# Kernel tuning notes

Hardware: AMD Instinct MI355X
Metric: run time of the kernel (lower is better)

## Reference

```python
import jax, jax.numpy as jnp
import numpy as np

B = 32768
SF = 40  # subframe_size


def _gru_cell(x, h, wih, whh):
    # PyTorch GRUCell (bias=False): gates ordered [r; z; n]
    gi = x @ wih.T
    gh = h @ whh.T
    ir, iz, inn = jnp.split(gi, 3, axis=-1)
    hr, hz, hn = jnp.split(gh, 3, axis=-1)
    r = jax.nn.sigmoid(ir + hr)
    z = jax.nn.sigmoid(iz + hz)
    n = jnp.tanh(inn + r * hn)
    return (1.0 - z) * n + z * h


def setup_inputs() -> dict:
    key = jax.random.key(0)
    ks = iter(jax.random.split(key, 32))

    def rn(shape, scale=None):
        s = scale if scale is not None else 1.0 / np.sqrt(shape[-1])
        return (jax.random.normal(next(ks), shape, dtype=jnp.float32) * s)

    inp = {
        'cond': rn((B, 80), 1.0),
        'prev_pred': rn((B, 256), 1.0),
        'exc_mem': rn((B, 256), 1.0),
        'period': 32.0 + 223.0 * jax.random.uniform(next(ks), (B,), dtype=jnp.float32),
        's1': rn((B, 160), 1.0),
        's2': rn((B, 128), 1.0),
        's3': rn((B, 128), 1.0),
        's4': rn((B, 164), 1.0),
        'w_gain': rn((1, 80)),
        'b_gain': jnp.zeros((1,), jnp.float32),
        'w_fwc0': rn((192, 328)),
        'w_fwc0_glu': rn((192, 192)),
        'wih1': rn((480, 272)),
        'whh1': rn((480, 160)),
        'wglu1': rn((160, 160)),
        'wih2': rn((384, 240)),
        'whh2': rn((384, 128)),
        'wglu2': rn((128, 128)),
        'wih3': rn((384, 208)),
        'whh3': rn((384, 128)),
        'wglu3': rn((128, 128)),
        'w_skip': rn((128, 688)),
        'w_skip_glu': rn((128, 128)),
        'w_sig': rn((40, 128)),
        'w_pg': rn((4, 192)),
        'b_pg': jnp.zeros((4,), jnp.float32),
    }
    return inp


def reference(cond, prev_pred, exc_mem, period, s1, s2, s3, s4,
              w_gain, b_gain, w_fwc0, w_fwc0_glu,
              wih1, whh1, wglu1, wih2, whh2, wglu2, wih3, whh3, wglu3,
              w_skip, w_skip_glu, w_sig, w_pg, b_pg):
    # eval mode (training=False): quantization noise is identity; compat_mode=False path
    dt = cond.dtype
    period = jnp.clip(jnp.nan_to_num(period, nan=128.0, posinf=128.0, neginf=128.0), 32.0, 255.0)
    rng = jnp.arange(SF + 4, dtype=dt)
    # fractional pitch lookup with linear interpolation into exc_mem
    idxf = 256.0 - period[:, None] + rng[None, :] - 2.0  # [B, SF+4]
    idx0 = jnp.floor(idxf)
    alpha = jnp.clip(idxf - idx0, 0.0, 1.0)
    W = exc_mem.shape[1]
    i0 = jnp.mod(jnp.clip(idx0, 0.0, 255.0).astype(jnp.int32), W)
    i1 = jnp.mod(jnp.clip(idx0 + 1.0, 0.0, 255.0).astype(jnp.int32), W)
    v0 = jnp.take_along_axis(exc_mem, i0, axis=1)
    v1 = jnp.take_along_axis(exc_mem, i1, axis=1)
    pred = (1.0 - alpha) * v0 + alpha * v1  # [B, SF+4]

    # bounded gain
    gain = 0.2 + 0.8 * jax.nn.sigmoid(cond @ w_gain.T + b_gain)
    gain = jnp.clip(jnp.nan_to_num(gain, nan=1.0, posinf=20.0, neginf=1e-3), 1e-3, 20.0)
    inv = 1.0 / (1e-5 + gain)
    pred_n = pred * inv
    prev = exc_mem[:, -SF:] * inv
    tmp = jnp.concatenate([cond, pred_n, prev], axis=1)  # [B, 164]
    fpitch = pred_n[:, 2:-2]  # [B, SF]

    # FWConv: linear over cat(state, x), tanh, GLU
    xcat = jnp.concatenate([s4, tmp], axis=1)  # [B, 328]
    fw = jnp.tanh(xcat @ w_fwc0.T)
    fwc0_out = fw * jax.nn.sigmoid(fw @ w_fwc0_glu.T)  # [B, 192]
    new_s4 = tmp

    pitch_gain = jax.nn.sigmoid(fwc0_out @ w_pg.T + b_pg)  # [B, 4]

    h1 = _gru_cell(jnp.concatenate([fwc0_out, pitch_gain[:, 0:1] * fpitch, prev], 1), s1, wih1, whh1)
    g1 = h1 * jax.nn.sigmoid(h1 @ wglu1.T)
    h2 = _gru_cell(jnp.concatenate([g1, pitch_gain[:, 1:2] * fpitch, prev], 1), s2, wih2, whh2)
    g2 = h2 * jax.nn.sigmoid(h2 @ wglu2.T)
    h3 = _gru_cell(jnp.concatenate([g2, pitch_gain[:, 2:3] * fpitch, prev], 1), s3, wih3, whh3)
    g3 = h3 * jax.nn.sigmoid(h3 @ wglu3.T)

    skip_in = jnp.concatenate([g1, g2, g3, fwc0_out, pitch_gain[:, 3:4] * fpitch, prev], 1)  # [B, 688]
    sk = jnp.tanh(skip_in @ w_skip.T)
    sk = sk * jax.nn.sigmoid(sk @ w_skip_glu.T)
    sig_out = jnp.tanh(sk @ w_sig.T) * gain  # [B, SF]

    exc_mem_new = jnp.concatenate([exc_mem[:, SF:], sig_out], 1)
    prev_pred_new = jnp.concatenate([prev_pred[:, SF:], pred[:, 2:2 + SF]], 1)
    return sig_out, exc_mem_new, prev_pred_new, h1, h2, h3, new_s4
```

## Files before the change

kernel.cpp:

```cpp
#include <hip/hip_runtime.h>
#include <hip/hip_bf16.h>
#include <cstdint>
#include <cmath>

#define BTOT 32768L
#define OSIG 0L
#define OEXC (BTOT*40L)
#define OPREV (OEXC + BTOT*256L)
#define OH1 (OPREV + BTOT*256L)
#define OH2 (OH1 + BTOT*160L)
#define OH3 (OH2 + BTOT*128L)
#define ONS4 (OH3 + BTOT*128L)

typedef __attribute__((ext_vector_type(8))) short short8;
typedef __attribute__((ext_vector_type(4))) short short4v;
typedef __attribute__((ext_vector_type(4))) float f32x4;

#define AP 968

#define W_F0     0L
#define W_F0G    67584L
#define W_PG     104448L
#define W_IH1R   107520L
#define W_IH1Z   162816L
#define W_IH1N   218112L
#define W_HH1R   273408L
#define W_HH1Z   310272L
#define W_HH1N   347136L
#define W_GLU1   384000L
#define W_IH2R   420864L
#define W_IH2Z   453632L
#define W_IH2N   486400L
#define W_HH2R   519168L
#define W_HH2Z   535552L
#define W_HH2N   551936L
#define W_GLU2   568320L
#define W_IH3R   584704L
#define W_IH3Z   613376L
#define W_IH3N   642048L
#define W_HH3R   670720L
#define W_HH3Z   687104L
#define W_HH3N   703488L
#define W_GLU3   719872L
#define W_SKIP   736256L
#define W_SKIPG  859136L
#define W_SIG    875520L

__device__ __forceinline__ float sigm(float x){ return 1.0f/(1.0f+__expf(-x)); }
__device__ __forceinline__ float tanh_f(float x){
    float e = __expf(2.0f*x);
    return 1.0f - 2.0f/(e+1.0f);
}
__device__ __forceinline__ uint16_t f2bf(float x){
    __hip_bfloat16 h = __float2bfloat16(x);
    return *(uint16_t*)&h;
}
__device__ __forceinline__ float bf2f(uint16_t h){
    union { float f; uint32_t u; } v; v.u = ((uint32_t)h)<<16;
    return v.f;
}
__device__ __forceinline__ short4v pack4(float4 v){
    short4v r;
    r.x=(short)f2bf(v.x); r.y=(short)f2bf(v.y); r.z=(short)f2bf(v.z); r.w=(short)f2bf(v.w);
    return r;
}

struct PrepArgs { const float* s[15]; };

__global__ __launch_bounds__(64) void prep_kernel(PrepArgs pa, uint16_t* dst){
    static const long J[27][8] = {
        {0,  0,192,328,352,192, W_F0,   0},
        {1,  0,192,192,192,192, W_F0G,  0},
        {13, 0,  4,192,192, 16, W_PG,   0},
        {2,  0,160,272,288,192, W_IH1R, 0},
        {2,160,160,272,288,192, W_IH1Z, 0},
        {2,320,160,272,288,192, W_IH1N, 0},
        {3,  0,160,160,192,192, W_HH1R, 0},
        {3,160,160,160,192,192, W_HH1Z, 0},
        {3,320,160,160,192,192, W_HH1N, 0},
        {4,  0,160,160,192,192, W_GLU1, 0},
        {5,  0,128,240,256,128, W_IH2R, 0},
        {5,128,128,240,256,128, W_IH2Z, 0},
        {5,256,128,240,256,128, W_IH2N, 0},
        {6,  0,128,128,128,128, W_HH2R, 0},
        {6,128,128,128,128,128, W_HH2Z, 0},
        {6,256,128,128,128,128, W_HH2N, 0},
        {7,  0,128,128,128,128, W_GLU2, 0},
        {8,  0,128,208,224,128, W_IH3R, 0},
        {8,128,128,208,224,128, W_IH3Z, 0},
        {8,256,128,208,224,128, W_IH3N, 0},
        {9,  0,128,128,128,128, W_HH3R, 0},
        {9,128,128,128,128,128, W_HH3Z, 0},
        {9,256,128,128,128,128, W_HH3N, 0},
        {10, 0,128,128,128,128, W_GLU3, 0},
        {11, 0,128,688,960,128, W_SKIP, 1},
        {12, 0,128,128,128,128, W_SKIPG,0},
        {14, 0, 40,128,128, 64, W_SIG,  0},
    };
    long row = blockIdx.x;
    int j = 0;
    while (row >= J[j][5]) { row -= J[j][5]; ++j; }
    const float* src = pa.s[J[j][0]];
    const long ro = J[j][1], N = J[j][2], K = J[j][3], KP = J[j][4];
    const int type = (int)J[j][7];
    uint16_t* d = dst + J[j][6] + row*KP;
    for (long k = threadIdx.x; k < KP; k += 64){
        float v = 0.0f;
        if (row < N){
            if (type == 0){
                if (k < K) v = src[(ro+row)*K + k];
            } else {
                long s = -1;
                if (k < 192) s = 416 + k;
                else if (k >= 232 && k < 272) s = 648 + (k-232);
                else if (k >= 288 && k < 448) s = (k-288);
                else if (k >= 544 && k < 672) s = 160 + (k-544);
                else if (k >= 768 && k < 896) s = 288 + (k-768);
                else if (k >= 896 && k < 936) s = 608 + (k-896);
                if (s >= 0) v = src[row*688 + s];
            }
        }
        d[k] = f2bf(v);
    }
}

template<int KS, int CNT>
__device__ __forceinline__ void wgemm4(f32x4 (&acc)[CNT][2],
    const uint16_t* __restrict__ Bw, int KP,
    const uint16_t* A, int P, int w, int r16, int g)
{
    constexpr int T = KS*CNT;
    constexpr int PF = (T < 6) ? T : 6;
    const uint16_t* ap = A + r16*P + g*8;
    const uint16_t* bbase = Bw + (size_t)(w*16 + r16)*KP + g*8;
    short8 ring[PF];
    #pragma unroll
    for (int t=0;t<PF;++t)
        ring[t] = *(const short8*)(bbase + (size_t)(t%CNT)*64*KP + (size_t)(t/CNT)*32);
    short8 af[2];
    #pragma unroll
    for (int t=0;t<T;++t){
        const int s = t/CNT, i = t%CNT;
        if (i==0){
            #pragma unroll
            for (int mt=0;mt<2;++mt) af[mt] = *(const short8*)(ap + mt*16*P + s*32);
        }
        short8 bf = ring[t%PF];
        if (t+PF < T)
            ring[t%PF] = *(const short8*)(bbase + (size_t)((t+PF)%CNT)*64*KP + (size_t)((t+PF)/CNT)*32);
        #pragma unroll
        for (int mt=0;mt<2;++mt)
            acc[i][mt] = __builtin_amdgcn_mfma_f32_16x16x32_bf16(af[mt], bf, acc[i][mt],0,0,0);
    }
}
template<int CNT> __device__ __forceinline__ void zacc(f32x4 (&a)[CNT][2]){
    f32x4 z4 = {0.f,0.f,0.f,0.f};
    #pragma unroll
    for (int i=0;i<CNT;++i){
        #pragma unroll
        for (int mt=0;mt<2;++mt) a[i][mt]=z4;
    }
}

__device__ __forceinline__ void gru1_h(const uint16_t* __restrict__ W, uint16_t* ACTp,
    const float* __restrict__ s1g, float* __restrict__ out,
    float (&hk)[3][2][4], int row0, int w, int r16, int g)
{
    f32x4 gx[3][2], gh[3][2], ra[3][2], za[3][2];
    zacc(gx); zacc(gh); zacc(ra); zacc(za);
    wgemm4<9,3>(gx, W+W_IH1N, 288, ACTp,     AP, w,r16,g);
    wgemm4<9,3>(ra, W+W_IH1R, 288, ACTp,     AP, w,r16,g);
    wgemm4<9,3>(za, W+W_IH1Z, 288, ACTp,     AP, w,r16,g);
    wgemm4<6,3>(gh, W+W_HH1N, 192, ACTp+544, AP, w,r16,g);
    wgemm4<6,3>(ra, W+W_HH1R, 192, ACTp+544, AP, w,r16,g);
    wgemm4<6,3>(za, W+W_HH1Z, 192, ACTp+544, AP, w,r16,g);
    #pragma unroll
    for (int i=0;i<3;++i){
        int n = (w+4*i)*16 + r16;
        #pragma unroll
        for (int mt=0;mt<2;++mt){
            #pragma unroll
            for (int q=0;q<4;++q){
                int mrow = mt*16+g*4+q;
                float h = 0.f;
                if (n < 160){
                    float hpv = s1g[(long)(row0+mrow)*160 + n];
                    float r = sigm(ra[i][mt][q]);
                    float z = sigm(za[i][mt][q]);
                    float nn = tanh_f(gx[i][mt][q] + r*gh[i][mt][q]);
                    h = (1.f-z)*nn + z*hpv;
                    out[OH1 + (long)(row0+mrow)*160 + n] = h;
                }
                hk[i][mt][q] = h;
                ACTp[mrow*AP+768+n] = f2bf(h);
            }
        }
    }
}
__device__ __forceinline__ void glu1(const uint16_t* __restrict__ W, uint16_t* ACTp,
                                     float (&hk)[3][2][4], int w, int r16, int g){
    f32x4 gl[3][2];
    zacc(gl);
    wgemm4<6,3>(gl, W+W_GLU1, 192, ACTp+768, AP, w,r16,g);
    #pragma unroll
    for (int i=0;i<3;++i){
        int n = (w+4*i)*16 + r16;
        if (n < 160){
            #pragma unroll
            for (int mt=0;mt<2;++mt)
                #pragma unroll
                for (int q=0;q<4;++q){
                    int mrow = mt*16+g*4+q;
                    ACTp[mrow*AP + 288 + n] = f2bf(hk[i][mt][q]*sigm(gl[i][mt][q]));
                }
        }
    }
}

template<int KSX, int KSH>
__device__ __forceinline__ void gru23_h(
    const uint16_t* __restrict__ Wxr, const uint16_t* __restrict__ Wxz, const uint16_t* __restrict__ Wxn, int KPX,
    const uint16_t* __restrict__ Whr, const uint16_t* __restrict__ Whz, const uint16_t* __restrict__ Whn, int KPH,
    const uint16_t* XA, const uint16_t* HA, int HAP,
    const float* __restrict__ sg, float* __restrict__ outp, long obase,
    uint16_t* HBdst, int HBpitch,
    float (&hk)[2][2][4], int row0, int w, int r16, int g)
{
    f32x4 gx[2][2], gh[2][2], ra[2][2], za[2][2];
    zacc(gx); zacc(gh); zacc(ra); zacc(za);
    wgemm4<KSX,2>(gx, Wxn, KPX, XA, AP, w,r16,g);
    wgemm4<KSX,2>(ra, Wxr, KPX, XA, AP, w,r16,g);
    wgemm4<KSX,2>(za, Wxz, KPX, XA, AP, w,r16,g);
    wgemm4<KSH,2>(gh, Whn, KPH, HA, HAP, w,r16,g);
    wgemm4<KSH,2>(ra, Whr, KPH, HA, HAP, w,r16,g);
    wgemm4<KSH,2>(za, Whz, KPH, HA, HAP, w,r16,g);
    #pragma unroll
    for (int i=0;i<2;++i){
        int n = (w+4*i)*16 + r16;
        #pragma unroll
        for (int mt=0;mt<2;++mt){
            #pragma unroll
            for (int q=0;q<4;++q){
                int mrow = mt*16+g*4+q;
                float hpv = sg[(long)(row0+mrow)*128 + n];
                float r = sigm(ra[i][mt][q]), z = sigm(za[i][mt][q]);
                float nn = tanh_f(gx[i][mt][q] + r*gh[i][mt][q]);
                float h = (1.f-z)*nn + z*hpv;
                outp[obase + (long)(row0+mrow)*128 + n] = h;
                hk[i][mt][q] = h;
                if (HBdst) HBdst[mrow*HBpitch + n] = f2bf(h);
            }
        }
    }
}

extern "C" __global__ __launch_bounds__(256, 2)
void fargan_mfma(const float* __restrict__ cond, const float* __restrict__ prev_pred,
                 const float* __restrict__ exc_mem, const float* __restrict__ period,
                 const float* __restrict__ s1, const float* __restrict__ s2,
                 const float* __restrict__ s3, const float* __restrict__ s4,
                 const float* __restrict__ w_gain, const float* __restrict__ b_gain,
                 const float* __restrict__ b_pg,
                 const uint16_t* __restrict__ W, float* __restrict__ out)
{
    __shared__ __align__(16) uint16_t ACT[32*AP];
    __shared__ __align__(16) uint16_t SH[32*136];
    __shared__ uint16_t FPITCHb[32*40];
    __shared__ float GAIN[32];
    __shared__ float PGs[32][4];

    const int tid = threadIdx.x;
    const int row0 = blockIdx.x * 32;
    const int w = tid >> 6, l = tid & 63, r16 = l & 15, g = l >> 4;
    const int rr = tid >> 3, c8 = tid & 7;
    const long grow = row0 + rr;

    const float* exc_row = exc_mem + grow*256;

    float a0 = 0.f;
    {
        const float4* c4 = (const float4*)(cond + grow*80);
        const float4* g4 = (const float4*)w_gain;
        float4* on4 = (float4*)(out + ONS4 + grow*164);
        for (int i=c8;i<20;i+=8){
            float4 cv = c4[i], gv = g4[i];
            a0 += cv.x*gv.x + cv.y*gv.y + cv.z*gv.z + cv.w*gv.w;
            *(short4v*)&ACT[rr*AP + 164 + 4*i] = pack4(cv);
            on4[i] = cv;
        }
    }
    a0 += __shfl_xor(a0,4,8); a0 += __shfl_xor(a0,2,8); a0 += __shfl_xor(a0,1,8);
    float gn = 0.2f + 0.8f*sigm(a0 + b_gain[0]);
    if (!(gn==gn)) gn = 1.0f;
    gn = fminf(fmaxf(gn, 0.001f), 20.0f);
    float inv = 1.0f/(1e-5f+gn);
    if (c8==0) GAIN[rr] = gn;

    float p = period[grow];
    p = (fabsf(p) <= 3.0e38f) ? p : 128.0f;
    p = fminf(fmaxf(p, 32.0f), 255.0f);

    for (int e=c8;e<44;e+=8){
        float idxf = 254.0f - p + (float)e;
        float idx0 = floorf(idxf);
        float al = fminf(fmaxf(idxf-idx0, 0.f), 1.f);
        int i0 = (int)fminf(fmaxf(idx0, 0.f), 255.f);
        int i1 = (int)fminf(fmaxf(idx0+1.f, 0.f), 255.f);
        float pr = (1.f-al)*exc_row[i0] + al*exc_row[i1];
        float pn = pr*inv;
        ACT[rr*AP + 244 + e] = f2bf(pn);
        out[ONS4 + grow*164 + 80 + e] = pn;
        if (e>=2 && e<42){
            out[OPREV + grow*256 + 216 + (e-2)] = pr;
            FPITCHb[rr*40 + (e-2)] = f2bf(pn);
        }
    }
    {
        const float4* pv4 = (const float4*)(exc_row + 216);
        float4* onp = (float4*)(out + ONS4 + grow*164 + 124);
        for (int i=c8;i<10;i+=8){
            float4 v = pv4[i];
            v.x*=inv; v.y*=inv; v.z*=inv; v.w*=inv;
            *(short4v*)&ACT[rr*AP + 288 + 4*i] = pack4(v);
            onp[i] = v;
        }
    }
    {
        const float4* s44 = (const float4*)(s4 + grow*164);
        for (int i=c8;i<41;i+=8)
            *(short4v*)&ACT[rr*AP + 4*i] = pack4(s44[i]);
        const float4* s14 = (const float4*)(s1 + grow*160);
        for (int i=c8;i<40;i+=8)
            *(short4v*)&ACT[rr*AP + 544 + 4*i] = pack4(s14[i]);
    }
    for (int i=328+c8;i<352;i+=8) ACT[rr*AP + i] = 0;
    for (int i=704+c8;i<736;i+=8) ACT[rr*AP + i] = 0;
    {
        const float4* pp4 = (const float4*)(prev_pred + grow*256 + 40);
        const float4* ex4 = (const float4*)(exc_row + 40);
        float4* op4 = (float4*)(out + OPREV + grow*256);
        float4* oe4 = (float4*)(out + OEXC + grow*256);
        for (int i=c8;i<54;i+=8){ op4[i] = pp4[i]; oe4[i] = ex4[i]; }
    }
    __syncthreads();

    float fwk[3][2][4];

    {
        f32x4 av[3][2]; zacc(av);
        wgemm4<11,3>(av, W+W_F0, 352, ACT, AP, w,r16,g);
        #pragma unroll
        for (int i=0;i<3;++i){
            int n = (w+4*i)*16 + r16;
            #pragma unroll
            for (int mt=0;mt<2;++mt)
                #pragma unroll
                for (int q=0;q<4;++q){
                    int mrow = mt*16+g*4+q;
                    float t = tanh_f(av[i][mt][q]);
                    fwk[i][mt][q] = t;
                    ACT[mrow*AP+352+n] = f2bf(t);
                }
        }
    }
    __syncthreads();

    {
        f32x4 av[3][2]; zacc(av);
        wgemm4<6,3>(av, W+W_F0G, 192, ACT+352, AP, w,r16,g);
        #pragma unroll
        for (int i=0;i<3;++i){
            int n = (w+4*i)*16 + r16;
            #pragma unroll
            for (int mt=0;mt<2;++mt)
                #pragma unroll
                for (int q=0;q<4;++q){
                    int mrow = mt*16+g*4+q;
                    ACT[mrow*AP+n] = f2bf(fwk[i][mt][q]*sigm(av[i][mt][q]));
                }
        }
    }
    __syncthreads();

    {
        f32x4 av[1][2]; zacc(av);
        wgemm4<6,1>(av, W+W_PG, 192, ACT, AP, 0, r16, g);
        if (w==0 && r16<4){
            float bp = b_pg[r16];
            #pragma unroll
            for (int mt=0;mt<2;++mt)
                #pragma unroll
                for (int q=0;q<4;++q)
                    PGs[mt*16+g*4+q][r16] = sigm(av[0][mt][q] + bp);
        }
    }
    __syncthreads();

    for (int i=c8;i<40;i+=8){
        ACT[rr*AP+192+i] = f2bf(PGs[rr][0]*bf2f(FPITCHb[rr*40+i]));
        ACT[rr*AP+232+i] = ACT[rr*AP+288+i];
    }
    __syncthreads();

    float hk1[3][2][4];
    gru1_h(W, ACT, s1, out, hk1, row0, w,r16,g);
    __syncthreads();

    glu1(W, ACT, hk1, w,r16,g);
    {
        const float4* s24 = (const float4*)(s2 + grow*128);
        for (int i=c8;i<32;i+=8)
            *(short4v*)&ACT[rr*AP + 544 + 4*i] = pack4(s24[i]);
    }
    for (int i=c8;i<40;i+=8){
        ACT[rr*AP+448+i] = f2bf(PGs[rr][1]*bf2f(FPITCHb[rr*40+i]));
        ACT[rr*AP+488+i] = ACT[rr*AP+232+i];
    }
    for (int i=528+c8;i<544;i+=8) ACT[rr*AP+i] = 0;
    __syncthreads();

    float hk[2][2][4];
    gru23_h<8,4>(W+W_IH2R, W+W_IH2Z, W+W_IH2N, 256,
                 W+W_HH2R, W+W_HH2Z, W+W_HH2N, 128,
                 ACT+288, ACT+544, AP, s2, out, OH2,
                 ACT+768, AP, hk, row0, w,r16,g);
    __syncthreads();

    {
        f32x4 gl[2][2]; zacc(gl);
        wgemm4<4,2>(gl, W+W_GLU2, 128, ACT+768, AP, w,r16,g);
        #pragma unroll
        for (int i=0;i<2;++i){
            int n = (w+4*i)*16 + r16;
            #pragma unroll
            for (int mt=0;mt<2;++mt)
                #pragma unroll
                for (int q=0;q<4;++q){
                    int mrow = mt*16+g*4+q;
                    ACT[mrow*AP+544+n] = f2bf(hk[i][mt][q]*sigm(gl[i][mt][q]));
                }
        }
    }
    {
        const float4* s34 = (const float4*)(s3 + grow*128);
        for (int i=c8;i<32;i+=8)
            *(short4v*)&SH[rr*136 + 4*i] = pack4(s34[i]);
    }
    for (int i=c8;i<40;i+=8){
        ACT[rr*AP+672+i] = f2bf(PGs[rr][2]*bf2f(FPITCHb[rr*40+i]));
        ACT[rr*AP+712+i] = ACT[rr*AP+232+i];
    }
    for (int i=752+c8;i<768;i+=8) ACT[rr*AP+i] = 0;
    __syncthreads();

    gru23_h<7,4>(W+W_IH3R, W+W_IH3Z, W+W_IH3N, 224,
                 W+W_HH3R, W+W_HH3Z, W+W_HH3N, 128,
                 ACT+544, SH, 136, s3, out, OH3,
                 (uint16_t*)nullptr, 0, hk, row0, w,r16,g);
    __syncthreads();

    #pragma unroll
    for (int i=0;i<2;++i){
        int n = (w+4*i)*16 + r16;
        #pragma unroll
        for (int mt=0;mt<2;++mt)
            #pragma unroll
            for (int q=0;q<4;++q)
                SH[(mt*16+g*4+q)*136 + n] = f2bf(hk[i][mt][q]);
    }
    __syncthreads();

    {
        f32x4 gl[2][2]; zacc(gl);
        wgemm4<4,2>(gl, W+W_GLU3, 128, SH, 136, w,r16,g);
        #pragma unroll
        for (int i=0;i<2;++i){
            int n = (w+4*i)*16 + r16;
            #pragma unroll
            for (int mt=0;mt<2;++mt)
                #pragma unroll
                for (int q=0;q<4;++q){
                    int mrow = mt*16+g*4+q;
                    ACT[mrow*AP+768+n] = f2bf(hk[i][mt][q]*sigm(gl[i][mt][q]));
                }
        }
    }
    for (int i=c8;i<40;i+=8)
        ACT[rr*AP+896+i] = f2bf(PGs[rr][3]*bf2f(FPITCHb[rr*40+i]));
    __syncthreads();

    float skk[2][2][4];
    {
        f32x4 av[2][2]; zacc(av);
        wgemm4<30,2>(av, W+W_SKIP, 960, ACT, AP, w,r16,g);
        #pragma unroll
        for (int i=0;i<2;++i){
            int n = (w+4*i)*16 + r16;
            #pragma unroll
            for (int mt=0;mt<2;++mt)
                #pragma unroll
                for (int q=0;q<4;++q){
                    int mrow = mt*16+g*4+q;
                    float t = tanh_f(av[i][mt][q]);
                    skk[i][mt][q] = t;
                    SH[mrow*136+n] = f2bf(t);
                }
        }
    }
    __syncthreads();
    {
        f32x4 av[2][2]; zacc(av);
        wgemm4<4,2>(av, W+W_SKIPG, 128, SH, 136, w,r16,g);
        #pragma unroll
        for (int i=0;i<2;++i){
            int n = (w+4*i)*16 + r16;
            #pragma unroll
            for (int mt=0;mt<2;++mt)
                #pragma unroll
                for (int q=0;q<4;++q){
                    int mrow = mt*16+g*4+q;
                    ACT[mrow*AP+n] = f2bf(skk[i][mt][q]*sigm(av[i][mt][q]));
                }
        }
    }
    __syncthreads();
    {
        f32x4 av[1][2]; zacc(av);
        wgemm4<4,1>(av, W+W_SIG, 128, ACT, AP, w,r16,g);
        int n = w*16 + r16;
        if (n < 40){
            #pragma unroll
            for (int mt=0;mt<2;++mt)
                #pragma unroll
                for (int q=0;q<4;++q){
                    int mrow = mt*16+g*4+q;
                    float sv = tanh_f(av[0][mt][q]) * GAIN[mrow];
                    out[OSIG + (long)(row0+mrow)*40 + n] = sv;
                    out[OEXC + (long)(row0+mrow)*256 + 216 + n] = sv;
                }
        }
    }
}

extern "C" void kernel_launch(void* const* d_in, const int* in_sizes, int n_in,
                              void* d_out, int out_size, void* d_ws, size_t ws_size,
                              hipStream_t stream) {
    const float* cond      = (const float*)d_in[0];
    const float* prev_pred = (const float*)d_in[1];
    const float* exc_mem   = (const float*)d_in[2];
    const float* period    = (const float*)d_in[3];
    const float* s1        = (const float*)d_in[4];
    const float* s2        = (const float*)d_in[5];
    const float* s3        = (const float*)d_in[6];
    const float* s4        = (const float*)d_in[7];
    const float* w_gain    = (const float*)d_in[8];
    const float* b_gain    = (const float*)d_in[9];
    const float* w_fwc0    = (const float*)d_in[10];
    const float* w_fwc0_glu= (const float*)d_in[11];
    const float* wih1      = (const float*)d_in[12];
    const float* whh1      = (const float*)d_in[13];
    const float* wglu1     = (const float*)d_in[14];
    const float* wih2      = (const float*)d_in[15];
    const float* whh2      = (const float*)d_in[16];
    const float* wglu2     = (const float*)d_in[17];
    const float* wih3      = (const float*)d_in[18];
    const float* whh3      = (const float*)d_in[19];
    const float* wglu3     = (const float*)d_in[20];
    const float* w_skip    = (const float*)d_in[21];
    const float* w_skip_glu= (const float*)d_in[22];
    const float* w_sig     = (const float*)d_in[23];
    const float* w_pg      = (const float*)d_in[24];
    const float* b_pg      = (const float*)d_in[25];
    float* out = (float*)d_out;
    uint16_t* wsbf = (uint16_t*)d_ws;

    PrepArgs pa;
    pa.s[0]=w_fwc0; pa.s[1]=w_fwc0_glu; pa.s[2]=wih1; pa.s[3]=whh1; pa.s[4]=wglu1;
    pa.s[5]=wih2; pa.s[6]=whh2; pa.s[7]=wglu2; pa.s[8]=wih3; pa.s[9]=whh3;
    pa.s[10]=wglu3; pa.s[11]=w_skip; pa.s[12]=w_skip_glu; pa.s[13]=w_pg; pa.s[14]=w_sig;

    hipLaunchKernelGGL(prep_kernel, dim3(3856), dim3(64), 0, stream, pa, wsbf);
    hipLaunchKernelGGL(fargan_mfma, dim3(1024), dim3(256), 0, stream,
        cond, prev_pred, exc_mem, period, s1, s2, s3, s4,
        w_gain, b_gain, b_pg, wsbf, out);
}
```

Baseline: 261.9 us.

## Switch to 32x32x16 MFMA with 64-row tiles and 512-thread blocks

Replaces the 16x16x32 MFMA GEMM helper with 32x32x16 bf16 MFMA tiles, doubles rows per block to 64 and threads to 512 (8 waves split by M-half and N-column). The three GRU gate GEMMs share one A-fragment load (wg3), and activations needed by the GLU steps are re-read from LDS instead of kept in registers. This is meant to halve weight traffic per row and raise MFMA efficiency. The cost is much larger LDS per block (about 130 KB), the loss of the B-prefetch ring, and uneven work across waves in the 192-wide stages.

```diff
diff --git a/kernel.cpp b/kernel.cpp
--- a/kernel.cpp
+++ b/kernel.cpp
@@ -14,37 +14,37 @@
 
 typedef __attribute__((ext_vector_type(8))) short short8;
 typedef __attribute__((ext_vector_type(4))) short short4v;
-typedef __attribute__((ext_vector_type(4))) float f32x4;
+typedef __attribute__((ext_vector_type(16))) float f32x16;
 
 #define AP 968
 
 #define W_F0     0L
 #define W_F0G    67584L
 #define W_PG     104448L
-#define W_IH1R   107520L
-#define W_IH1Z   162816L
-#define W_IH1N   218112L
-#define W_HH1R   273408L
-#define W_HH1Z   310272L
-#define W_HH1N   347136L
-#define W_GLU1   384000L
-#define W_IH2R   420864L
-#define W_IH2Z   453632L
-#define W_IH2N   486400L
-#define W_HH2R   519168L
-#define W_HH2Z   535552L
-#define W_HH2N   551936L
-#define W_GLU2   568320L
-#define W_IH3R   584704L
-#define W_IH3Z   613376L
-#define W_IH3N   642048L
-#define W_HH3R   670720L
-#define W_HH3Z   687104L
-#define W_HH3N   703488L
-#define W_GLU3   719872L
-#define W_SKIP   736256L
-#define W_SKIPG  859136L
-#define W_SIG    875520L
+#define W_IH1R   110592L
+#define W_IH1Z   165888L
+#define W_IH1N   221184L
+#define W_HH1R   276480L
+#define W_HH1Z   313344L
+#define W_HH1N   350208L
+#define W_GLU1   387072L
+#define W_IH2R   423936L
+#define W_IH2Z   456704L
+#define W_IH2N   489472L
+#define W_HH2R   522240L
+#define W_HH2Z   538624L
+#define W_HH2N   555008L
+#define W_GLU2   571392L
+#define W_IH3R   587776L
+#define W_IH3Z   616448L
+#define W_IH3N   645120L
+#define W_HH3R   673792L
+#define W_HH3Z   690176L
+#define W_HH3N   706560L
+#define W_GLU3   722944L
+#define W_SKIP   739328L
+#define W_SKIPG  862208L
+#define W_SIG    878592L
 
 __device__ __forceinline__ float sigm(float x){ return 1.0f/(1.0f+__expf(-x)); }
 __device__ __forceinline__ float tanh_f(float x){
@@ -64,6 +64,10 @@
     r.x=(short)f2bf(v.x); r.y=(short)f2bf(v.y); r.z=(short)f2bf(v.z); r.w=(short)f2bf(v.w);
     return r;
 }
+__device__ __forceinline__ void z16(f32x16 &a){
+    #pragma unroll
+    for (int i=0;i<16;++i) a[i]=0.f;
+}
 
 struct PrepArgs { const float* s[15]; };
 
@@ -71,7 +75,7 @@
     static const long J[27][8] = {
         {0,  0,192,328,352,192, W_F0,   0},
         {1,  0,192,192,192,192, W_F0G,  0},
-        {13, 0,  4,192,192, 16, W_PG,   0},
+        {13, 0,  4,192,192, 32, W_PG,   0},
         {2,  0,160,272,288,192, W_IH1R, 0},
         {2,160,160,272,288,192, W_IH1Z, 0},
         {2,320,160,272,288,192, W_IH1N, 0},
@@ -124,137 +128,51 @@
     }
 }
 
-template<int KS, int CNT>
-__device__ __forceinline__ void wgemm4(f32x4 (&acc)[CNT][2],
-    const uint16_t* __restrict__ Bw, int KP,
-    const uint16_t* A, int P, int w, int r16, int g)
+template<int KS, int NT>
+__device__ __forceinline__ void wg1(f32x16 (&acc)[NT],
+    const uint16_t* __restrict__ B, int KP,
+    const uint16_t* A, int P, int mt, int nb, int c32, int hl)
 {
-    constexpr int T = KS*CNT;
-    constexpr int PF = (T < 6) ? T : 6;
-    const uint16_t* ap = A + r16*P + g*8;
-    const uint16_t* bbase = Bw + (size_t)(w*16 + r16)*KP + g*8;
-    short8 ring[PF];
+    const uint16_t* ap = A + (mt*32 + c32)*P + hl*8;
+    const uint16_t* bp = B + (size_t)(nb + c32)*KP + hl*8;
     #pragma unroll
-    for (int t=0;t<PF;++t)
-        ring[t] = *(const short8*)(bbase + (size_t)(t%CNT)*64*KP + (size_t)(t/CNT)*32);
-    short8 af[2];
+    for (int s=0;s<KS;++s){
+        short8 a = *(const short8*)(ap + s*16);
+        #pragma unroll
+        for (int i=0;i<NT;++i){
+            short8 b = *(const short8*)(bp + (size_t)(i*128)*KP + s*16);
+            acc[i] = __builtin_amdgcn_mfma_f32_32x32x16_bf16(a, b, acc[i], 0,0,0);
+        }
+    }
+}
+template<int KS, int NT>
+__device__ __forceinline__ void wg3(f32x16 (&a0)[NT], f32x16 (&a1)[NT], f32x16 (&a2)[NT],
+    const uint16_t* __restrict__ B0, const uint16_t* __restrict__ B1,
+    const uint16_t* __restrict__ B2, int KP,
+    const uint16_t* A, int P, int mt, int nb, int c32, int hl)
+{
+    const uint16_t* ap = A + (mt*32 + c32)*P + hl*8;
+    const size_t boff = (size_t)(nb + c32)*KP + hl*8;
+    const uint16_t* b0 = B0 + boff;
+    const uint16_t* b1 = B1 + boff;
+    const uint16_t* b2 = B2 + boff;
     #pragma unroll
-    for (int t=0;t<T;++t){
-        const int s = t/CNT, i = t%CNT;
-        if (i==0){
-            #pragma unroll
-            for (int mt=0;mt<2;++mt) af[mt] = *(const short8*)(ap + mt*16*P + s*32);
-        }
-        short8 bf = ring[t%PF];
-        if (t+PF < T)
-            ring[t%PF] = *(const short8*)(bbase + (size_t)((t+PF)%CNT)*64*KP + (size_t)((t+PF)/CNT)*32);
-        #pragma unroll
-        for (int mt=0;mt<2;++mt)
-            acc[i][mt] = __builtin_amdgcn_mfma_f32_16x16x32_bf16(af[mt], bf, acc[i][mt],0,0,0);
-    }
-}
-template<int CNT> __device__ __forceinline__ void zacc(f32x4 (&a)[CNT][2]){
-    f32x4 z4 = {0.f,0.f,0.f,0.f};
-    #pragma unroll
-    for (int i=0;i<CNT;++i){
-        #pragma unroll
-        for (int mt=0;mt<2;++mt) a[i][mt]=z4;
-    }
-}
-
-__device__ __forceinline__ void gru1_h(const uint16_t* __restrict__ W, uint16_t* ACTp,
-    const float* __restrict__ s1g, float* __restrict__ out,
-    float (&hk)[3][2][4], int row0, int w, int r16, int g)
-{
-    f32x4 gx[3][2], gh[3][2], ra[3][2], za[3][2];
-    zacc(gx); zacc(gh); zacc(ra); zacc(za);
-    wgemm4<9,3>(gx, W+W_IH1N, 288, ACTp,     AP, w,r16,g);
-    wgemm4<9,3>(ra, W+W_IH1R, 288, ACTp,     AP, w,r16,g);
-    wgemm4<9,3>(za, W+W_IH1Z, 288, ACTp,     AP, w,r16,g);
-    wgemm4<6,3>(gh, W+W_HH1N, 192, ACTp+544, AP, w,r16,g);
-    wgemm4<6,3>(ra, W+W_HH1R, 192, ACTp+544, AP, w,r16,g);
-    wgemm4<6,3>(za, W+W_HH1Z, 192, ACTp+544, AP, w,r16,g);
-    #pragma unroll
-    for (int i=0;i<3;++i){
-        int n = (w+4*i)*16 + r16;
-        #pragma unroll
-        for (int mt=0;mt<2;++mt){
-            #pragma unroll
-            for (int q=0;q<4;++q){
-                int mrow = mt*16+g*4+q;
-                float h = 0.f;
-                if (n < 160){
-                    float hpv = s1g[(long)(row0+mrow)*160 + n];
-                    float r = sigm(ra[i][mt][q]);
-                    float z = sigm(za[i][mt][q]);
-                    float nn = tanh_f(gx[i][mt][q] + r*gh[i][mt][q]);
-                    h = (1.f-z)*nn + z*hpv;
-                    out[OH1 + (long)(row0+mrow)*160 + n] = h;
-                }
-                hk[i][mt][q] = h;
-                ACTp[mrow*AP+768+n] = f2bf(h);
-            }
-        }
-    }
-}
-__device__ __forceinline__ void glu1(const uint16_t* __restrict__ W, uint16_t* ACTp,
-                                     float (&hk)[3][2][4], int w, int r16, int g){
-    f32x4 gl[3][2];
-    zacc(gl);
-    wgemm4<6,3>(gl, W+W_GLU1, 192, ACTp+768, AP, w,r16,g);
-    #pragma unroll
-    for (int i=0;i<3;++i){
-        int n = (w+4*i)*16 + r16;
-        if (n < 160){
-            #pragma unroll
-            for (int mt=0;mt<2;++mt)
-                #pragma unroll
-                for (int q=0;q<4;++q){
-                    int mrow = mt*16+g*4+q;
-                    ACTp[mrow*AP + 288 + n] = f2bf(hk[i][mt][q]*sigm(gl[i][mt][q]));
-                }
-        }
-    }
-}
-
-template<int KSX, int KSH>
-__device__ __forceinline__ void gru23_h(
-    const uint16_t* __restrict__ Wxr, const uint16_t* __restrict__ Wxz, const uint16_t* __restrict__ Wxn, int KPX,
-    const uint16_t* __restrict__ Whr, const uint16_t* __restrict__ Whz, const uint16_t* __restrict__ Whn, int KPH,
-    const uint16_t* XA, const uint16_t* HA, int HAP,
-    const float* __restrict__ sg, float* __restrict__ outp, long obase,
-    uint16_t* HBdst, int HBpitch,
-    float (&hk)[2][2][4], int row0, int w, int r16, int g)
-{
-    f32x4 gx[2][2], gh[2][2], ra[2][2], za[2][2];
-    zacc(gx); zacc(gh); zacc(ra); zacc(za);
-    wgemm4<KSX,2>(gx, Wxn, KPX, XA, AP, w,r16,g);
-    wgemm4<KSX,2>(ra, Wxr, KPX, XA, AP, w,r16,g);
-    wgemm4<KSX,2>(za, Wxz, KPX, XA, AP, w,r16,g);
-    wgemm4<KSH,2>(gh, Whn, KPH, HA, HAP, w,r16,g);
-    wgemm4<KSH,2>(ra, Whr, KPH, HA, HAP, w,r16,g);
-    wgemm4<KSH,2>(za, Whz, KPH, HA, HAP, w,r16,g);
-    #pragma unroll
-    for (int i=0;i<2;++i){
-        int n = (w+4*i)*16 + r16;
-        #pragma unroll
-        for (int mt=0;mt<2;++mt){
-            #pragma unroll
-            for (int q=0;q<4;++q){
-                int mrow = mt*16+g*4+q;
-                float hpv = sg[(long)(row0+mrow)*128 + n];
-                float r = sigm(ra[i][mt][q]), z = sigm(za[i][mt][q]);
-                float nn = tanh_f(gx[i][mt][q] + r*gh[i][mt][q]);
-                float h = (1.f-z)*nn + z*hpv;
-                outp[obase + (long)(row0+mrow)*128 + n] = h;
-                hk[i][mt][q] = h;
-                if (HBdst) HBdst[mrow*HBpitch + n] = f2bf(h);
-            }
-        }
-    }
-}
-
-extern "C" __global__ __launch_bounds__(256, 2)
+    for (int s=0;s<KS;++s){
+        short8 a = *(const short8*)(ap + s*16);
+        #pragma unroll
+        for (int i=0;i<NT;++i){
+            const size_t o = (size_t)(i*128)*KP + s*16;
+            short8 f0 = *(const short8*)(b0 + o);
+            short8 f1 = *(const short8*)(b1 + o);
+            short8 f2 = *(const short8*)(b2 + o);
+            a0[i] = __builtin_amdgcn_mfma_f32_32x32x16_bf16(a, f0, a0[i], 0,0,0);
+            a1[i] = __builtin_amdgcn_mfma_f32_32x32x16_bf16(a, f1, a1[i], 0,0,0);
+            a2[i] = __builtin_amdgcn_mfma_f32_32x32x16_bf16(a, f2, a2[i], 0,0,0);
+        }
+    }
+}
+
+extern "C" __global__ __launch_bounds__(512, 2)
 void fargan_mfma(const float* __restrict__ cond, const float* __restrict__ prev_pred,
                  const float* __restrict__ exc_mem, const float* __restrict__ period,
                  const float* __restrict__ s1, const float* __restrict__ s2,
@@ -263,15 +181,17 @@
                  const float* __restrict__ b_pg,
                  const uint16_t* __restrict__ W, float* __restrict__ out)
 {
-    __shared__ __align__(16) uint16_t ACT[32*AP];
-    __shared__ __align__(16) uint16_t SH[32*136];
-    __shared__ uint16_t FPITCHb[32*40];
-    __shared__ float GAIN[32];
-    __shared__ float PGs[32][4];
+    __shared__ __align__(16) uint16_t ACT[64*AP];
+    __shared__ __align__(16) uint16_t SH[64*136];
+    __shared__ uint16_t FPITCHb[64*40];
+    __shared__ float GAIN[64];
+    __shared__ float PGs[64][4];
 
     const int tid = threadIdx.x;
-    const int row0 = blockIdx.x * 32;
-    const int w = tid >> 6, l = tid & 63, r16 = l & 15, g = l >> 4;
+    const int row0 = blockIdx.x * 64;
+    const int w = tid >> 6, l = tid & 63;
+    const int c32 = l & 31, hl = l >> 5;
+    const int mt = w & 1, nb = (w >> 1) * 32;
     const int rr = tid >> 3, c8 = tid & 7;
     const long grow = row0 + rr;
 
@@ -344,54 +264,70 @@
     }
     __syncthreads();
 
-    float fwk[3][2][4];
-
-    {
-        f32x4 av[3][2]; zacc(av);
-        wgemm4<11,3>(av, W+W_F0, 352, ACT, AP, w,r16,g);
-        #pragma unroll
-        for (int i=0;i<3;++i){
-            int n = (w+4*i)*16 + r16;
+    f32x16 fwk[2];
+
+    if (w < 4){
+        f32x16 av[2]; z16(av[0]); z16(av[1]);
+        wg1<22,2>(av, W+W_F0, 352, ACT, AP, mt, nb, c32, hl);
+        #pragma unroll
+        for (int i=0;i<2;++i){
+            int n = nb + i*128 + c32;
             #pragma unroll
-            for (int mt=0;mt<2;++mt)
-                #pragma unroll
-                for (int q=0;q<4;++q){
-                    int mrow = mt*16+g*4+q;
-                    float t = tanh_f(av[i][mt][q]);
-                    fwk[i][mt][q] = t;
-                    ACT[mrow*AP+352+n] = f2bf(t);
-                }
-        }
-    }
-    __syncthreads();
-
-    {
-        f32x4 av[3][2]; zacc(av);
-        wgemm4<6,3>(av, W+W_F0G, 192, ACT+352, AP, w,r16,g);
-        #pragma unroll
-        for (int i=0;i<3;++i){
-            int n = (w+4*i)*16 + r16;
+            for (int r=0;r<16;++r){
+                int mrow = mt*32 + (r&3) + 8*(r>>2) + 4*hl;
+                float t = tanh_f(av[i][r]);
+                fwk[i][r] = t;
+                ACT[mrow*AP+352+n] = f2bf(t);
+            }
+        }
+    } else {
+        f32x16 av[1]; z16(av[0]);
+        wg1<22,1>(av, W+W_F0, 352, ACT, AP, mt, nb, c32, hl);
+        int n = nb + c32;
+        #pragma unroll
+        for (int r=0;r<16;++r){
+            int mrow = mt*32 + (r&3) + 8*(r>>2) + 4*hl;
+            float t = tanh_f(av[0][r]);
+            fwk[0][r] = t;
+            ACT[mrow*AP+352+n] = f2bf(t);
+        }
+    }
+    __syncthreads();
+
+    if (w < 4){
+        f32x16 av[2]; z16(av[0]); z16(av[1]);
+        wg1<12,2>(av, W+W_F0G, 192, ACT+352, AP, mt, nb, c32, hl);
+        #pragma unroll
+        for (int i=0;i<2;++i){
+            int n = nb + i*128 + c32;
             #pragma unroll
-            for (int mt=0;mt<2;++mt)
-                #pragma unroll
-                for (int q=0;q<4;++q){
-                    int mrow = mt*16+g*4+q;
-                    ACT[mrow*AP+n] = f2bf(fwk[i][mt][q]*sigm(av[i][mt][q]));
-                }
-        }
-    }
-    __syncthreads();
-
-    {
-        f32x4 av[1][2]; zacc(av);
-        wgemm4<6,1>(av, W+W_PG, 192, ACT, AP, 0, r16, g);
-        if (w==0 && r16<4){
-            float bp = b_pg[r16];
+            for (int r=0;r<16;++r){
+                int mrow = mt*32 + (r&3) + 8*(r>>2) + 4*hl;
+                ACT[mrow*AP+n] = f2bf(fwk[i][r]*sigm(av[i][r]));
+            }
+        }
+    } else {
+        f32x16 av[1]; z16(av[0]);
+        wg1<12,1>(av, W+W_F0G, 192, ACT+352, AP, mt, nb, c32, hl);
+        int n = nb + c32;
+        #pragma unroll
+        for (int r=0;r<16;++r){
+            int mrow = mt*32 + (r&3) + 8*(r>>2) + 4*hl;
+            ACT[mrow*AP+n] = f2bf(fwk[0][r]*sigm(av[0][r]));
+        }
+    }
+    __syncthreads();
+
+    if (w < 2){
+        f32x16 pv[1]; z16(pv[0]);
+        wg1<12,1>(pv, W+W_PG, 192, ACT, AP, w, 0, c32, hl);
+        if (c32 < 4){
+            float bp = b_pg[c32];
             #pragma unroll
-            for (int mt=0;mt<2;++mt)
-                #pragma unroll
-                for (int q=0;q<4;++q)
-                    PGs[mt*16+g*4+q][r16] = sigm(av[0][mt][q] + bp);
+            for (int r=0;r<16;++r){
+                int mrow = w*32 + (r&3) + 8*(r>>2) + 4*hl;
+                PGs[mrow][c32] = sigm(pv[0][r] + bp);
+            }
         }
     }
     __syncthreads();
@@ -402,11 +338,81 @@
     }
     __syncthreads();
 
-    float hk1[3][2][4];
-    gru1_h(W, ACT, s1, out, hk1, row0, w,r16,g);
-    __syncthreads();
-
-    glu1(W, ACT, hk1, w,r16,g);
+    if (w < 4){
+        f32x16 gx[2], gh[2], ra[2], za[2];
+        z16(gx[0]); z16(gx[1]); z16(gh[0]); z16(gh[1]);
+        z16(ra[0]); z16(ra[1]); z16(za[0]); z16(za[1]);
+        wg3<18,2>(gx, ra, za, W+W_IH1N, W+W_IH1R, W+W_IH1Z, 288, ACT,     AP, mt, nb, c32, hl);
+        wg3<12,2>(gh, ra, za, W+W_HH1N, W+W_HH1R, W+W_HH1Z, 192, ACT+544, AP, mt, nb, c32, hl);
+        #pragma unroll
+        for (int i=0;i<2;++i){
+            int n = nb + i*128 + c32;
+            #pragma unroll
+            for (int r=0;r<16;++r){
+                int mrow = mt*32 + (r&3) + 8*(r>>2) + 4*hl;
+                float h = 0.f;
+                if (n < 160){
+                    float hpv = s1[(long)(row0+mrow)*160 + n];
+                    float rv = sigm(ra[i][r]);
+                    float z = sigm(za[i][r]);
+                    float nn = tanh_f(gx[i][r] + rv*gh[i][r]);
+                    h = (1.f-z)*nn + z*hpv;
+                    out[OH1 + (long)(row0+mrow)*160 + n] = h;
+                }
+                ACT[mrow*AP+768+n] = f2bf(h);
+            }
+        }
+    } else {
+        f32x16 gx[1], gh[1], ra[1], za[1];
+        z16(gx[0]); z16(gh[0]); z16(ra[0]); z16(za[0]);
+        wg3<18,1>(gx, ra, za, W+W_IH1N, W+W_IH1R, W+W_IH1Z, 288, ACT,     AP, mt, nb, c32, hl);
+        wg3<12,1>(gh, ra, za, W+W_HH1N, W+W_HH1R, W+W_HH1Z, 192, ACT+544, AP, mt, nb, c32, hl);
+        int n = nb + c32;
+        #pragma unroll
+        for (int r=0;r<16;++r){
+            int mrow = mt*32 + (r&3) + 8*(r>>2) + 4*hl;
+            float h = 0.f;
+            if (n < 160){
+                float hpv = s1[(long)(row0+mrow)*160 + n];
+                float rv = sigm(ra[0][r]);
+                float z = sigm(za[0][r]);
+                float nn = tanh_f(gx[0][r] + rv*gh[0][r]);
+                h = (1.f-z)*nn + z*hpv;
+                out[OH1 + (long)(row0+mrow)*160 + n] = h;
+            }
+            ACT[mrow*AP+768+n] = f2bf(h);
+        }
+    }
+    __syncthreads();
+
+    if (w < 4){
+        f32x16 gl[2]; z16(gl[0]); z16(gl[1]);
+        wg1<12,2>(gl, W+W_GLU1, 192, ACT+768, AP, mt, nb, c32, hl);
+        #pragma unroll
+        for (int i=0;i<2;++i){
+            int n = nb + i*128 + c32;
+            if (n < 160){
+                #pragma unroll
+                for (int r=0;r<16;++r){
+                    int mrow = mt*32 + (r&3) + 8*(r>>2) + 4*hl;
+                    float h = bf2f(ACT[mrow*AP+768+n]);
+                    ACT[mrow*AP+288+n] = f2bf(h*sigm(gl[i][r]));
+                }
+            }
+        }
+    } else {
+        f32x16 gl[1]; z16(gl[0]);
+        wg1<12,1>(gl, W+W_GLU1, 192, ACT+768, AP, mt, nb, c32, hl);
+        int n = nb + c32;
+        if (n < 160){
+            #pragma unroll
+            for (int r=0;r<16;++r){
+                int mrow = mt*32 + (r&3) + 8*(r>>2) + 4*hl;
+                float h = bf2f(ACT[mrow*AP+768+n]);
+                ACT[mrow*AP+288+n] = f2bf(h*sigm(gl[0][r]));
+            }
+        }
+    }
     {
         const float4* s24 = (const float4*)(s2 + grow*128);
         for (int i=c8;i<32;i+=8)
@@ -419,26 +425,34 @@
     for (int i=528+c8;i<544;i+=8) ACT[rr*AP+i] = 0;
     __syncthreads();
 
-    float hk[2][2][4];
-    gru23_h<8,4>(W+W_IH2R, W+W_IH2Z, W+W_IH2N, 256,
-                 W+W_HH2R, W+W_HH2Z, W+W_HH2N, 128,
-                 ACT+288, ACT+544, AP, s2, out, OH2,
-                 ACT+768, AP, hk, row0, w,r16,g);
-    __syncthreads();
-
-    {
-        f32x4 gl[2][2]; zacc(gl);
-        wgemm4<4,2>(gl, W+W_GLU2, 128, ACT+768, AP, w,r16,g);
-        #pragma unroll
-        for (int i=0;i<2;++i){
-            int n = (w+4*i)*16 + r16;
-            #pragma unroll
-            for (int mt=0;mt<2;++mt)
-                #pragma unroll
-                for (int q=0;q<4;++q){
-                    int mrow = mt*16+g*4+q;
-                    ACT[mrow*AP+544+n] = f2bf(hk[i][mt][q]*sigm(gl[i][mt][q]));
-                }
+    {
+        f32x16 gx[1], gh[1], ra[1], za[1];
+        z16(gx[0]); z16(gh[0]); z16(ra[0]); z16(za[0]);
+        wg3<16,1>(gx, ra, za, W+W_IH2N, W+W_IH2R, W+W_IH2Z, 256, ACT+288, AP, mt, nb, c32, hl);
+        wg3<8,1>(gh, ra, za, W+W_HH2N, W+W_HH2R, W+W_HH2Z, 128, ACT+544, AP, mt, nb, c32, hl);
+        int n = nb + c32;
+        #pragma unroll
+        for (int r=0;r<16;++r){
+            int mrow = mt*32 + (r&3) + 8*(r>>2) + 4*hl;
+            float hpv = s2[(long)(row0+mrow)*128 + n];
+            float rv = sigm(ra[0][r]), z = sigm(za[0][r]);
+            float nn = tanh_f(gx[0][r] + rv*gh[0][r]);
+            float h = (1.f-z)*nn + z*hpv;
+            out[OH2 + (long)(row0+mrow)*128 + n] = h;
+            ACT[mrow*AP+768+n] = f2bf(h);
+        }
+    }
+    __syncthreads();
+
+    {
+        f32x16 gl[1]; z16(gl[0]);
+        wg1<8,1>(gl, W+W_GLU2, 128, ACT+768, AP, mt, nb, c32, hl);
+        int n = nb + c32;
+        #pragma unroll
+        for (int r=0;r<16;++r){
+            int mrow = mt*32 + (r&3) + 8*(r>>2) + 4*hl;
+            float h = bf2f(ACT[mrow*AP+768+n]);
+            ACT[mrow*AP+544+n] = f2bf(h*sigm(gl[0][r]));
         }
     }
     {
@@ -453,91 +467,86 @@
     for (int i=752+c8;i<768;i+=8) ACT[rr*AP+i] = 0;
     __syncthreads();
 
-    gru23_h<7,4>(W+W_IH3R, W+W_IH3Z, W+W_IH3N, 224,
-                 W+W_HH3R, W+W_HH3Z, W+W_HH3N, 128,
-                 ACT+544, SH, 136, s3, out, OH3,
-                 (uint16_t*)nullptr, 0, hk, row0, w,r16,g);
-    __syncthreads();
-
-    #pragma unroll
-    for (int i=0;i<2;++i){
-        int n = (w+4*i)*16 + r16;
-        #pragma unroll
-        for (int mt=0;mt<2;++mt)
-            #pragma unroll
-            for (int q=0;q<4;++q)
-                SH[(mt*16+g*4+q)*136 + n] = f2bf(hk[i][mt][q]);
-    }
-    __syncthreads();
-
-    {
-        f32x4 gl[2][2]; zacc(gl);
-        wgemm4<4,2>(gl, W+W_GLU3, 128, SH, 136, w,r16,g);
-        #pragma unroll
-        for (int i=0;i<2;++i){
-            int n = (w+4*i)*16 + r16;
-            #pragma unroll
-            for (int mt=0;mt<2;++mt)
-                #pragma unroll
-                for (int q=0;q<4;++q){
-                    int mrow = mt*16+g*4+q;
-                    ACT[mrow*AP+768+n] = f2bf(hk[i][mt][q]*sigm(gl[i][mt][q]));
-                }
+    f32x16 hk3;
+    {
+        f32x16 gx[1], gh[1], ra[1], za[1];
+        z16(gx[0]); z16(gh[0]); z16(ra[0]); z16(za[0]);
+        wg3<14,1>(gx, ra, za, W+W_IH3N, W+W_IH3R, W+W_IH3Z, 224, ACT+544, AP, mt, nb, c32, hl);
+        wg3<8,1>(gh, ra, za, W+W_HH3N, W+W_HH3R, W+W_HH3Z, 128, SH, 136, mt, nb, c32, hl);
+        int n = nb + c32;
+        #pragma unroll
+        for (int r=0;r<16;++r){
+            int mrow = mt*32 + (r&3) + 8*(r>>2) + 4*hl;
+            float hpv = s3[(long)(row0+mrow)*128 + n];
+            float rv = sigm(ra[0][r]), z = sigm(za[0][r]);
+            float nn = tanh_f(gx[0][r] + rv*gh[0][r]);
+            float h = (1.f-z)*nn + z*hpv;
+            out[OH3 + (long)(row0+mrow)*128 + n] = h;
+            hk3[r] = h;
+        }
+    }
+    __syncthreads();
+
+    {
+        int n = nb + c32;
+        #pragma unroll
+        for (int r=0;r<16;++r){
+            int mrow = mt*32 + (r&3) + 8*(r>>2) + 4*hl;
+            SH[mrow*136 + n] = f2bf(hk3[r]);
+        }
+    }
+    __syncthreads();
+
+    {
+        f32x16 gl[1]; z16(gl[0]);
+        wg1<8,1>(gl, W+W_GLU3, 128, SH, 136, mt, nb, c32, hl);
+        int n = nb + c32;
+        #pragma unroll
+        for (int r=0;r<16;++r){
+            int mrow = mt*32 + (r&3) + 8*(r>>2) + 4*hl;
+            float h = bf2f(SH[mrow*136 + n]);
+            ACT[mrow*AP+768+n] = f2bf(h*sigm(gl[0][r]));
         }
     }
     for (int i=c8;i<40;i+=8)
         ACT[rr*AP+896+i] = f2bf(PGs[rr][3]*bf2f(FPITCHb[rr*40+i]));
     __syncthreads();
 
-    float skk[2][2][4];
-    {
-        f32x4 av[2][2]; zacc(av);
-        wgemm4<30,2>(av, W+W_SKIP, 960, ACT, AP, w,r16,g);
-        #pragma unroll
-        for (int i=0;i<2;++i){
-            int n = (w+4*i)*16 + r16;
-            #pragma unroll
-            for (int mt=0;mt<2;++mt)
-                #pragma unroll
-                for (int q=0;q<4;++q){
-                    int mrow = mt*16+g*4+q;
-                    float t = tanh_f(av[i][mt][q]);
-                    skk[i][mt][q] = t;
-                    SH[mrow*136+n] = f2bf(t);
-                }
-        }
-    }
-    __syncthreads();
-    {
-        f32x4 av[2][2]; zacc(av);
-        wgemm4<4,2>(av, W+W_SKIPG, 128, SH, 136, w,r16,g);
-        #pragma unroll
-        for (int i=0;i<2;++i){
-            int n = (w+4*i)*16 + r16;
-            #pragma unroll
-            for (int mt=0;mt<2;++mt)
-                #pragma unroll
-                for (int q=0;q<4;++q){
-                    int mrow = mt*16+g*4+q;
-                    ACT[mrow*AP+n] = f2bf(skk[i][mt][q]*sigm(av[i][mt][q]));
-                }
-        }
-    }
-    __syncthreads();
-    {
-        f32x4 av[1][2]; zacc(av);
-        wgemm4<4,1>(av, W+W_SIG, 128, ACT, AP, w,r16,g);
-        int n = w*16 + r16;
+    {
+        f32x16 av[1]; z16(av[0]);
+        wg1<60,1>(av, W+W_SKIP, 960, ACT, AP, mt, nb, c32, hl);
+        int n = nb + c32;
+        #pragma unroll
+        for (int r=0;r<16;++r){
+            int mrow = mt*32 + (r&3) + 8*(r>>2) + 4*hl;
+            SH[mrow*136+n] = f2bf(tanh_f(av[0][r]));
+        }
+    }
+    __syncthreads();
+    {
+        f32x16 av[1]; z16(av[0]);
+        wg1<8,1>(av, W+W_SKIPG, 128, SH, 136, mt, nb, c32, hl);
+        int n = nb + c32;
+        #pragma unroll
+        for (int r=0;r<16;++r){
+            int mrow = mt*32 + (r&3) + 8*(r>>2) + 4*hl;
+            float t = bf2f(SH[mrow*136+n]);
+            ACT[mrow*AP+n] = f2bf(t*sigm(av[0][r]));
+        }
+    }
+    __syncthreads();
+    if (w < 4){
+        f32x16 av[1]; z16(av[0]);
+        wg1<8,1>(av, W+W_SIG, 128, ACT, AP, mt, nb, c32, hl);
+        int n = nb + c32;
         if (n < 40){
             #pragma unroll
-            for (int mt=0;mt<2;++mt)
-                #pragma unroll
-                for (int q=0;q<4;++q){
-                    int mrow = mt*16+g*4+q;
-                    float sv = tanh_f(av[0][mt][q]) * GAIN[mrow];
-                    out[OSIG + (long)(row0+mrow)*40 + n] = sv;
-                    out[OEXC + (long)(row0+mrow)*256 + 216 + n] = sv;
-                }
+            for (int r=0;r<16;++r){
+                int mrow = mt*32 + (r&3) + 8*(r>>2) + 4*hl;
+                float sv = tanh_f(av[0][r]) * GAIN[mrow];
+                out[OSIG + (long)(row0+mrow)*40 + n] = sv;
+                out[OEXC + (long)(row0+mrow)*256 + 216 + n] = sv;
+            }
         }
     }
 }
@@ -579,8 +588,8 @@
     pa.s[5]=wih2; pa.s[6]=whh2; pa.s[7]=wglu2; pa.s[8]=wih3; pa.s[9]=whh3;
     pa.s[10]=wglu3; pa.s[11]=w_skip; pa.s[12]=w_skip_glu; pa.s[13]=w_pg; pa.s[14]=w_sig;
 
-    hipLaunchKernelGGL(prep_kernel, dim3(3856), dim3(64), 0, stream, pa, wsbf);
-    hipLaunchKernelGGL(fargan_mfma, dim3(1024), dim3(256), 0, stream,
+    hipLaunchKernelGGL(prep_kernel, dim3(3872), dim3(64), 0, stream, pa, wsbf);
+    hipLaunchKernelGGL(fargan_mfma, dim3(512), dim3(512), 0, stream,
         cond, prev_pred, exc_mem, period, s1, s2, s3, s4,
         w_gain, b_gain, b_pg, wsbf, out);
 }
```

After: 292.5 us. 11.7% more time.
